# Optimization experiments

Measured on AMD Instinct MI355X. Metric: run time of the kernel, lower is better.

The kernel has to match this reference:

```python
import jax, jax.numpy as jnp
import numpy as np

N = 100_000      # nodes
E = 1_600_000    # edges (avg degree 16)
P = 100_000      # pos/neg sampled edges
L = 3            # GIN layers
D_IN = 128
D_H = 128
D_MLP = 512
D_PRED = D_H // 2
D_FIN = 1


def setup_inputs() -> dict:
    key = jax.random.key(0)
    ks = jax.random.split(key, 12)
    s_in = 1.0 / np.sqrt(D_IN)
    s_mlp = 1.0 / np.sqrt(D_MLP)
    s_h = 1.0 / np.sqrt(D_H)
    s_p = 1.0 / np.sqrt(D_PRED)
    return {
        "x":   jax.random.normal(ks[0], (N, D_IN), jnp.float32),
        "W1":  jax.random.normal(ks[1], (L, D_IN, D_MLP), jnp.float32) * s_in,
        "b1":  jnp.zeros((L, D_MLP), jnp.float32),
        "W2":  jax.random.normal(ks[2], (L, D_MLP, D_H), jnp.float32) * s_mlp,
        "b2":  jnp.zeros((L, D_H), jnp.float32),
        "Wp1": jax.random.normal(ks[3], (D_H, D_PRED), jnp.float32) * s_h,
        "bp1": jnp.zeros((D_PRED,), jnp.float32),
        "Wp2": jax.random.normal(ks[4], (D_PRED, D_FIN), jnp.float32) * s_p,
        "bp2": jnp.zeros((D_FIN,), jnp.float32),
        "edge_src": jax.random.randint(ks[5], (E,), 0, N),
        "edge_dst": jax.random.randint(ks[6], (E,), 0, N),
        "pos_src": jax.random.randint(ks[7], (P,), 0, N),
        "pos_dst": jax.random.randint(ks[8], (P,), 0, N),
        "neg_src": jax.random.randint(ks[9], (P,), 0, N),
        "neg_dst": jax.random.randint(ks[10], (P,), 0, N),
    }


def reference(x, W1, b1, W2, b2, Wp1, bp1, Wp2, bp2,
              edge_src, edge_dst, pos_src, pos_dst, neg_src, neg_dst):
    h = x
    for l in range(L):
        # GINConv 'sum': aggregate neighbor features src->dst, eps=0
        agg = jax.ops.segment_sum(h[edge_src], edge_dst, num_segments=N)
        z = jax.nn.relu((h + agg) @ W1[l] + b1[l])   # [N, D_MLP]
        h = z @ W2[l] + b2[l]                        # [N, D_H]
        h = jax.nn.relu(h)                           # outer ReLU in forward()

    def predict(src, dst):
        z = jax.nn.relu((h[src] * h[dst]) @ Wp1 + bp1)
        return z @ Wp2 + bp2                         # [P, D_FIN]

    h_pos = predict(pos_src, pos_dst)
    h_neg = predict(neg_src, neg_dst)
    return (h_pos, h_neg, h)
```

## Files before the change

kernel.cpp:

```cpp
#include <hip/hip_runtime.h>

typedef unsigned short ushort_t;

constexpr int NN = 100000;
constexpr int EE = 1600000;
constexpr int PP = 100000;
constexpr int DH = 128;
constexpr int DM = 512;

using frag_b16 = __attribute__((ext_vector_type(8))) short;
using frag_f32 = __attribute__((ext_vector_type(4))) float;

union FragU {
  ushort_t s[8];
  uint4 u;
  frag_b16 f;
};

__device__ inline void split_bf16(float x, ushort_t& hi, ushort_t& lo) {
  unsigned int bx = __float_as_uint(x);
  hi = (ushort_t)(bx >> 16);
  float hf = __uint_as_float(bx & 0xFFFF0000u);
  float r = x - hf;
  unsigned int br = __float_as_uint(r);
  unsigned int rb = br + 0x7FFFu + ((br >> 16) & 1u);
  lo = (ushort_t)(rb >> 16);
}

__device__ inline ushort_t rne_bf16(float x) {
  unsigned int u = __float_as_uint(x);
  unsigned int r = u + 0x7FFFu + ((u >> 16) & 1u);
  return (ushort_t)(r >> 16);
}

__device__ inline void bf2x(unsigned int u, float& a, float& b) {
  a = __uint_as_float(u << 16);
  b = __uint_as_float(u & 0xFFFF0000u);
}

__device__ inline void ldrec(const ushort_t* __restrict__ wp, int tile, int lane, FragU& f) {
  f.u = *(const uint4*)(wp + ((size_t)(tile * 64 + lane)) * 8);
}


__global__ void hist_kernel(const int* __restrict__ dst, int* __restrict__ deg) {
  int i = blockIdx.x * 256 + threadIdx.x;
  if (i < EE) atomicAdd(&deg[dst[i]], 1);
}

__global__ void scan1_kernel(const int* __restrict__ deg, int* __restrict__ inc,
                             int* __restrict__ bsum) {
  __shared__ int buf[2][512];
  int base = blockIdx.x * 512;
  for (int i = threadIdx.x; i < 512; i += 256) {
    int g = base + i;
    buf[0][i] = (g < NN) ? deg[g] : 0;
  }
  __syncthreads();
  int cur = 0;
  for (int off = 1; off < 512; off <<= 1) {
    int nxt = cur ^ 1;
    for (int i = threadIdx.x; i < 512; i += 256) {
      int v = buf[cur][i];
      if (i >= off) v += buf[cur][i - off];
      buf[nxt][i] = v;
    }
    __syncthreads();
    cur = nxt;
  }
  for (int i = threadIdx.x; i < 512; i += 256) {
    int g = base + i;
    if (g < NN) inc[g] = buf[cur][i];
  }
  if (threadIdx.x == 0) bsum[blockIdx.x] = buf[cur][511];
}

__global__ void scan2_kernel(int* __restrict__ bsum, int nb) {
  __shared__ int buf[2][256];
  int i = threadIdx.x;
  buf[0][i] = (i < nb) ? bsum[i] : 0;
  __syncthreads();
  int cur = 0;
  for (int off = 1; off < 256; off <<= 1) {
    int nxt = cur ^ 1;
    int v = buf[cur][i];
    if (i >= off) v += buf[cur][i - off];
    buf[nxt][i] = v;
    __syncthreads();
    cur = nxt;
  }
  if (i < nb) bsum[i] = (i == 0) ? 0 : buf[cur][i - 1];
}

__global__ void scan3_kernel(const int* __restrict__ inc, const int* __restrict__ deg,
                             const int* __restrict__ bsum,
                             int* __restrict__ row_off, int* __restrict__ cursor) {
  int i = blockIdx.x * 256 + threadIdx.x;
  if (i < NN) {
    int excl = inc[i] - deg[i] + bsum[i >> 9];
    row_off[i] = excl;
    cursor[i] = excl;
    if (i == NN - 1) row_off[NN] = excl + deg[i];
  }
}

constexpr int SC_NW = 8;
constexpr int SC_WND = (NN + SC_NW - 1) / SC_NW;
constexpr int SC_EPB = 8192;
constexpr int SC_CHUNKS = (EE + SC_EPB - 1) / SC_EPB;

__global__ __launch_bounds__(256) void scatter_kernel(const int* __restrict__ esrc,
                                                      const int* __restrict__ edst,
                                                      int* __restrict__ cursor,
                                                      int* __restrict__ csr) {
  const int w = blockIdx.x & (SC_NW - 1);
  const int chunk = blockIdx.x / SC_NW;
  const int lo = w * SC_WND;
  const int hi = lo + SC_WND;
  const int base = chunk * SC_EPB;
  #pragma unroll 4
  for (int it = 0; it < SC_EPB / 256; ++it) {
    int i = base + it * 256 + threadIdx.x;
    if (i < EE) {
      int d = edst[i];
      if (d >= lo && d < hi) {
        int p = atomicAdd(&cursor[d], 1);
        csr[p] = esrc[i];
      }
    }
  }
}

__global__ void pack_w1_kernel(const float* __restrict__ W1, ushort_t* __restrict__ wp) {
  int t = blockIdx.x * 256 + threadIdx.x;
  if (t >= 3 * 128 * 64) return;
  int lane = t & 63;
  int tile = t >> 6;
  int tk = tile & 3;
  int tn = (tile >> 2) & 31;
  int layer = tile >> 7;
  int n = tn * 16 + (lane & 15);
  int k0 = tk * 32 + (lane >> 4) * 8;
  const float* src = W1 + (size_t)layer * DH * DM;
  size_t dst = (size_t)t * 8;
  #pragma unroll
  for (int j = 0; j < 8; ++j) wp[dst + j] = rne_bf16(src[(size_t)(k0 + j) * DM + n]);
}

__global__ void pack_w2_kernel(const float* __restrict__ W2, ushort_t* __restrict__ wp) {
  int t = blockIdx.x * 256 + threadIdx.x;
  if (t >= 3 * 128 * 64) return;
  int lane = t & 63;
  int tile = t >> 6;
  int tk = tile & 15;
  int tn = (tile >> 4) & 7;
  int layer = tile >> 7;
  int n = tn * 16 + (lane & 15);
  int k0 = tk * 32 + (lane >> 4) * 8;
  const float* src = W2 + (size_t)layer * DM * DH;
  size_t dst = (size_t)t * 8;
  #pragma unroll
  for (int j = 0; j < 8; ++j) wp[dst + j] = rne_bf16(src[(size_t)(k0 + j) * DH + n]);
}

__global__ void cvt_bf16_kernel(const float* __restrict__ x, ushort_t* __restrict__ xb) {
  int i = blockIdx.x * 256 + threadIdx.x;
  if (i < NN * DH / 4) {
    float4 v = ((const float4*)x)[i];
    ushort4 o;
    o.x = rne_bf16(v.x); o.y = rne_bf16(v.y); o.z = rne_bf16(v.z); o.w = rne_bf16(v.w);
    ((ushort4*)xb)[i] = o;
  }
}

__global__ __launch_bounds__(256) void agg_kernel(const ushort_t* __restrict__ hbf,
                                                  const int* __restrict__ row_off,
                                                  const int* __restrict__ csr,
                                                  ushort_t* __restrict__ s_hi,
                                                  ushort_t* __restrict__ s_lo) {
  int t = blockIdx.x * 256 + threadIdx.x;
  int grp = t >> 4;
  int lane = t & 15;
  if (grp >= NN) return;
  const uint4* hp = (const uint4*)hbf;
  float acc[8];
  {
    uint4 v = hp[(size_t)grp * 16 + lane];
    bf2x(v.x, acc[0], acc[1]);
    bf2x(v.y, acc[2], acc[3]);
    bf2x(v.z, acc[4], acc[5]);
    bf2x(v.w, acc[6], acc[7]);
  }
  int e = row_off[grp];
  int e1 = row_off[grp + 1];
  for (; e + 1 < e1; e += 2) {
    uint4 a = hp[(size_t)csr[e] * 16 + lane];
    uint4 b = hp[(size_t)csr[e + 1] * 16 + lane];
    float f0, f1;
    bf2x(a.x, f0, f1); acc[0] += f0; acc[1] += f1;
    bf2x(a.y, f0, f1); acc[2] += f0; acc[3] += f1;
    bf2x(a.z, f0, f1); acc[4] += f0; acc[5] += f1;
    bf2x(a.w, f0, f1); acc[6] += f0; acc[7] += f1;
    bf2x(b.x, f0, f1); acc[0] += f0; acc[1] += f1;
    bf2x(b.y, f0, f1); acc[2] += f0; acc[3] += f1;
    bf2x(b.z, f0, f1); acc[4] += f0; acc[5] += f1;
    bf2x(b.w, f0, f1); acc[6] += f0; acc[7] += f1;
  }
  if (e < e1) {
    uint4 a = hp[(size_t)csr[e] * 16 + lane];
    float f0, f1;
    bf2x(a.x, f0, f1); acc[0] += f0; acc[1] += f1;
    bf2x(a.y, f0, f1); acc[2] += f0; acc[3] += f1;
    bf2x(a.z, f0, f1); acc[4] += f0; acc[5] += f1;
    bf2x(a.w, f0, f1); acc[6] += f0; acc[7] += f1;
  }
  unsigned int hw[4], lw[4];
  #pragma unroll
  for (int i = 0; i < 4; ++i) {
    ushort_t h0, l0, h1, l1;
    split_bf16(acc[2 * i], h0, l0);
    split_bf16(acc[2 * i + 1], h1, l1);
    hw[i] = (unsigned int)h0 | ((unsigned int)h1 << 16);
    lw[i] = (unsigned int)l0 | ((unsigned int)l1 << 16);
  }
  size_t o = (size_t)grp * DH + lane * 8;
  *(uint4*)(s_hi + o) = make_uint4(hw[0], hw[1], hw[2], hw[3]);
  *(uint4*)(s_lo + o) = make_uint4(lw[0], lw[1], lw[2], lw[3]);
}

__global__ __launch_bounds__(128) void mlp_kernel(
    const ushort_t* __restrict__ s_hi, const ushort_t* __restrict__ s_lo,
    const ushort_t* __restrict__ w1p, const float* __restrict__ b1s,
    const ushort_t* __restrict__ w2p, const float* __restrict__ b2s,
    float* __restrict__ hout_f32, ushort_t* __restrict__ hout_bf16) {
  __shared__ float zt[64 * 66];
  const int tid = threadIdx.x;
  const int wave = tid >> 6;
  const int lane = tid & 63;
  const int quad = lane >> 4;
  const int l15 = lane & 15;
  const int m_base = wave * 32;
  const int row0 = blockIdx.x * 64;

  frag_b16 a_hi[2][4], a_lo[2][4];
  #pragma unroll
  for (int ms = 0; ms < 2; ++ms) {
    int gr = row0 + m_base + ms * 16 + l15;
    if (gr >= NN) gr = NN - 1;
    #pragma unroll
    for (int tk = 0; tk < 4; ++tk) {
      size_t o = (size_t)gr * DH + tk * 32 + quad * 8;
      FragU uh, ul;
      uh.u = *(const uint4*)(s_hi + o);
      ul.u = *(const uint4*)(s_lo + o);
      a_hi[ms][tk] = uh.f;
      a_lo[ms][tk] = ul.f;
    }
  }

  frag_f32 hacc[2][8];
  #pragma unroll
  for (int ms = 0; ms < 2; ++ms)
    #pragma unroll
    for (int tn = 0; tn < 8; ++tn) hacc[ms][tn] = {0.f, 0.f, 0.f, 0.f};

  for (int ch = 0; ch < 8; ++ch) {
    frag_f32 za[2][4];
    #pragma unroll
    for (int ms = 0; ms < 2; ++ms)
      #pragma unroll
      for (int tn = 0; tn < 4; ++tn) za[ms][tn] = {0.f, 0.f, 0.f, 0.f};

    FragU wb[2][4];
    #pragma unroll
    for (int tn = 0; tn < 4; ++tn) ldrec(w1p, ch * 16 + tn * 4, lane, wb[0][tn]);
    #pragma unroll
    for (int tk = 0; tk < 4; ++tk) {
      int cur = tk & 1, nxt = cur ^ 1;
      if (tk < 3) {
        #pragma unroll
        for (int tn = 0; tn < 4; ++tn)
          ldrec(w1p, ch * 16 + tn * 4 + tk + 1, lane, wb[nxt][tn]);
      }
      #pragma unroll
      for (int tn = 0; tn < 4; ++tn) {
        #pragma unroll
        for (int ms = 0; ms < 2; ++ms) {
          za[ms][tn] = __builtin_amdgcn_mfma_f32_16x16x32_bf16(a_hi[ms][tk], wb[cur][tn].f,
                                                               za[ms][tn], 0, 0, 0);
          za[ms][tn] = __builtin_amdgcn_mfma_f32_16x16x32_bf16(a_lo[ms][tk], wb[cur][tn].f,
                                                               za[ms][tn], 0, 0, 0);
        }
      }
    }

    #pragma unroll
    for (int tn = 0; tn < 4; ++tn) {
      float b1v = b1s[ch * 64 + tn * 16 + l15];
      #pragma unroll
      for (int ms = 0; ms < 2; ++ms) {
        float z0 = fmaxf(za[ms][tn][0] + b1v, 0.f);
        float z1 = fmaxf(za[ms][tn][1] + b1v, 0.f);
        float z2 = fmaxf(za[ms][tn][2] + b1v, 0.f);
        float z3 = fmaxf(za[ms][tn][3] + b1v, 0.f);
        float* zp = &zt[(tn * 16 + l15) * 66 + m_base + ms * 16 + quad * 4];
        *(float2*)zp = make_float2(z0, z1);
        *(float2*)(zp + 2) = make_float2(z2, z3);
      }
    }

    #pragma unroll
    for (int kt = 0; kt < 2; ++kt) {
      int ktg = ch * 2 + kt;
      FragU wb2[8];
      #pragma unroll
      for (int tn = 0; tn < 8; ++tn) ldrec(w2p, tn * 16 + ktg, lane, wb2[tn]);
      FragU zh[2], zl[2];
      #pragma unroll
      for (int ms = 0; ms < 2; ++ms) {
        #pragma unroll
        for (int j = 0; j < 8; ++j) {
          int k = kt * 32 + quad * 8 + j;
          float v = zt[k * 66 + m_base + ms * 16 + l15];
          split_bf16(v, zh[ms].s[j], zl[ms].s[j]);
        }
      }
      #pragma unroll
      for (int tn = 0; tn < 8; ++tn) {
        #pragma unroll
        for (int ms = 0; ms < 2; ++ms) {
          hacc[ms][tn] = __builtin_amdgcn_mfma_f32_16x16x32_bf16(zh[ms].f, wb2[tn].f,
                                                                 hacc[ms][tn], 0, 0, 0);
          hacc[ms][tn] = __builtin_amdgcn_mfma_f32_16x16x32_bf16(zl[ms].f, wb2[tn].f,
                                                                 hacc[ms][tn], 0, 0, 0);
        }
      }
    }
  }

  #pragma unroll
  for (int tn = 0; tn < 8; ++tn) {
    int col = tn * 16 + l15;
    float b2v = b2s[col];
    #pragma unroll
    for (int ms = 0; ms < 2; ++ms) {
      #pragma unroll
      for (int r = 0; r < 4; ++r) {
        int gr = row0 + m_base + ms * 16 + quad * 4 + r;
        if (gr < NN) {
          float v = fmaxf(hacc[ms][tn][r] + b2v, 0.f);
          if (hout_f32) hout_f32[(size_t)gr * DH + col] = v;
          if (hout_bf16) hout_bf16[(size_t)gr * DH + col] = rne_bf16(v);
        }
      }
    }
  }
}

__global__ __launch_bounds__(256) void predict_kernel(
    const float* __restrict__ h, const int* __restrict__ psrc, const int* __restrict__ pdst,
    const int* __restrict__ nsrc, const int* __restrict__ ndst,
    const float* __restrict__ Wp1, const float* __restrict__ bp1,
    const float* __restrict__ Wp2, const float* __restrict__ bp2,
    float* __restrict__ out) {
  __shared__ float g_tile[64 * 132];
  const int tid = threadIdx.x;
  const int s0 = blockIdx.x * 64;

  #pragma unroll
  for (int i = 0; i < 8; ++i) {
    int idx = tid + i * 256;
    int smp = s0 + (idx >> 5);
    int c4 = (idx & 31) << 2;
    float4 g = make_float4(0.f, 0.f, 0.f, 0.f);
    if (smp < 2 * PP) {
      int si = (smp < PP) ? psrc[smp] : nsrc[smp - PP];
      int di = (smp < PP) ? pdst[smp] : ndst[smp - PP];
      float4 a = *(const float4*)(h + (size_t)si * DH + c4);
      float4 b = *(const float4*)(h + (size_t)di * DH + c4);
      g = make_float4(a.x * b.x, a.y * b.y, a.z * b.z, a.w * b.w);
    }
    *(float4*)(&g_tile[(idx >> 5) * 132 + c4]) = g;
  }
  __syncthreads();

  const int tr = (tid >> 4) << 2;
  const int tc = (tid & 15) << 2;
  float z[4][4];
  #pragma unroll
  for (int r = 0; r < 4; ++r)
    #pragma unroll
    for (int c = 0; c < 4; ++c) z[r][c] = 0.f;

  for (int k = 0; k < DH; ++k) {
    float4 w = *(const float4*)(Wp1 + ((size_t)k << 6) + tc);
    float a[4];
    #pragma unroll
    for (int r = 0; r < 4; ++r) a[r] = g_tile[(tr + r) * 132 + k];
    #pragma unroll
    for (int r = 0; r < 4; ++r) {
      z[r][0] = fmaf(a[r], w.x, z[r][0]);
      z[r][1] = fmaf(a[r], w.y, z[r][1]);
      z[r][2] = fmaf(a[r], w.z, z[r][2]);
      z[r][3] = fmaf(a[r], w.w, z[r][3]);
    }
  }

  float4 b1v = *(const float4*)(bp1 + tc);
  float4 w2v = *(const float4*)(Wp2 + tc);
  float part[4];
  #pragma unroll
  for (int r = 0; r < 4; ++r) {
    part[r] = fmaxf(z[r][0] + b1v.x, 0.f) * w2v.x +
              fmaxf(z[r][1] + b1v.y, 0.f) * w2v.y +
              fmaxf(z[r][2] + b1v.z, 0.f) * w2v.z +
              fmaxf(z[r][3] + b1v.w, 0.f) * w2v.w;
  }
  #pragma unroll
  for (int off = 1; off < 16; off <<= 1) {
    #pragma unroll
    for (int r = 0; r < 4; ++r) part[r] += __shfl_xor(part[r], off, 64);
  }
  if ((tid & 15) == 0) {
    float bias = bp2[0];
    #pragma unroll
    for (int r = 0; r < 4; ++r) {
      int smp = s0 + tr + r;
      if (smp < 2 * PP) out[smp] = part[r] + bias;
    }
  }
}

extern "C" void kernel_launch(void* const* d_in, const int* in_sizes, int n_in,
                              void* d_out, int out_size, void* d_ws, size_t ws_size,
                              hipStream_t stream) {
  const float* x   = (const float*)d_in[0];
  const float* W1  = (const float*)d_in[1];
  const float* b1  = (const float*)d_in[2];
  const float* W2  = (const float*)d_in[3];
  const float* b2  = (const float*)d_in[4];
  const float* Wp1 = (const float*)d_in[5];
  const float* bp1 = (const float*)d_in[6];
  const float* Wp2 = (const float*)d_in[7];
  const float* bp2 = (const float*)d_in[8];
  const int* esrc = (const int*)d_in[9];
  const int* edst = (const int*)d_in[10];
  const int* psrc = (const int*)d_in[11];
  const int* pdst = (const int*)d_in[12];
  const int* nsrc = (const int*)d_in[13];
  const int* ndst = (const int*)d_in[14];

  float* out = (float*)d_out;
  float* out_pred = out;
  float* hbuf = out + 2 * (size_t)PP;
  ushort_t* hbf = (ushort_t*)hbuf;

  char* w = (char*)d_ws;
  ushort_t* s_hi = (ushort_t*)w;
  ushort_t* s_lo = s_hi + (size_t)NN * DH;
  ushort_t* w1p  = s_lo + (size_t)NN * DH;
  ushort_t* w2p  = w1p + 3 * 128 * 64 * 8;
  int* row_off = (int*)(w2p + 3 * 128 * 64 * 8);
  int* csr     = row_off + (NN + 1);
  int* deg    = (int*)w;
  int* inc    = deg + NN;
  int* bsum   = inc + NN;
  int* cursor = bsum + 256;

  hipMemsetAsync(deg, 0, NN * sizeof(int), stream);
  hist_kernel<<<(EE + 255) / 256, 256, 0, stream>>>(edst, deg);
  scan1_kernel<<<(NN + 511) / 512, 256, 0, stream>>>(deg, inc, bsum);
  scan2_kernel<<<1, 256, 0, stream>>>(bsum, (NN + 511) / 512);
  scan3_kernel<<<(NN + 255) / 256, 256, 0, stream>>>(inc, deg, bsum, row_off, cursor);
  scatter_kernel<<<SC_CHUNKS * SC_NW, 256, 0, stream>>>(esrc, edst, cursor, csr);

  pack_w1_kernel<<<96, 256, 0, stream>>>(W1, w1p);
  pack_w2_kernel<<<96, 256, 0, stream>>>(W2, w2p);

  cvt_bf16_kernel<<<(NN * DH / 4 + 255) / 256, 256, 0, stream>>>(x, hbf);

  for (int l = 0; l < 3; ++l) {
    agg_kernel<<<(NN * 16 + 255) / 256, 256, 0, stream>>>(hbf, row_off, csr, s_hi, s_lo);
    mlp_kernel<<<(NN + 63) / 64, 128, 0, stream>>>(
        s_hi, s_lo,
        w1p + (size_t)l * 128 * 64 * 8, b1 + (size_t)l * DM,
        w2p + (size_t)l * 128 * 64 * 8, b2 + (size_t)l * DH,
        (l == 2) ? hbuf : nullptr, (l == 2) ? nullptr : hbf);
  }

  predict_kernel<<<(2 * PP + 63) / 64, 256, 0, stream>>>(
      hbuf, psrc, pdst, nsrc, ndst, Wp1, bp1, Wp2, bp2, out_pred);
}
```

Before: 887.7 us.

## Stage MLP weight tiles in LDS via global_load_lds with 4-wave blocks

```diff
diff --git a/kernel.cpp b/kernel.cpp
--- a/kernel.cpp
+++ b/kernel.cpp
@@ -38,8 +38,10 @@
   b = __uint_as_float(u & 0xFFFF0000u);
 }
 
-__device__ inline void ldrec(const ushort_t* __restrict__ wp, int tile, int lane, FragU& f) {
-  f.u = *(const uint4*)(wp + ((size_t)(tile * 64 + lane)) * 8);
+__device__ inline void g2l16(const ushort_t* __restrict__ g, ushort_t* l) {
+  __builtin_amdgcn_global_load_lds(
+      (const __attribute__((address_space(1))) void*)g,
+      (__attribute__((address_space(3))) void*)l, 16, 0, 0);
 }
 
 
@@ -152,11 +154,11 @@
   if (t >= 3 * 128 * 64) return;
   int lane = t & 63;
   int tile = t >> 6;
-  int tk = tile & 15;
-  int tn = (tile >> 4) & 7;
+  int tn = tile & 7;
+  int ktg = (tile >> 3) & 15;
   int layer = tile >> 7;
   int n = tn * 16 + (lane & 15);
-  int k0 = tk * 32 + (lane >> 4) * 8;
+  int k0 = ktg * 32 + (lane >> 4) * 8;
   const float* src = W2 + (size_t)layer * DM * DH;
   size_t dst = (size_t)t * 8;
   #pragma unroll
@@ -228,19 +230,21 @@
   *(uint4*)(s_lo + o) = make_uint4(lw[0], lw[1], lw[2], lw[3]);
 }
 
-__global__ __launch_bounds__(128) void mlp_kernel(
+__global__ __launch_bounds__(256, 2) void mlp_kernel(
     const ushort_t* __restrict__ s_hi, const ushort_t* __restrict__ s_lo,
     const ushort_t* __restrict__ w1p, const float* __restrict__ b1s,
     const ushort_t* __restrict__ w2p, const float* __restrict__ b2s,
     float* __restrict__ hout_f32, ushort_t* __restrict__ hout_bf16) {
-  __shared__ float zt[64 * 66];
+  __shared__ ushort_t wA[8 * 512];
+  __shared__ ushort_t wB[8 * 512];
+  __shared__ float zt[32 * 130];
   const int tid = threadIdx.x;
   const int wave = tid >> 6;
   const int lane = tid & 63;
   const int quad = lane >> 4;
   const int l15 = lane & 15;
   const int m_base = wave * 32;
-  const int row0 = blockIdx.x * 64;
+  const int row0 = blockIdx.x * 128;
 
   frag_b16 a_hi[2][4], a_lo[2][4];
   #pragma unroll
@@ -264,78 +268,74 @@
     #pragma unroll
     for (int tn = 0; tn < 8; ++tn) hacc[ms][tn] = {0.f, 0.f, 0.f, 0.f};
 
-  for (int ch = 0; ch < 8; ++ch) {
-    frag_f32 za[2][4];
+  for (int ch = 0; ch < 16; ++ch) {
+    #pragma unroll
+    for (int i = 0; i < 2; ++i)
+      g2l16(w1p + ((size_t)(ch * 512 + i * 256 + tid)) * 8, wA + (i * 256 + tid) * 8);
+    #pragma unroll
+    for (int i = 0; i < 2; ++i)
+      g2l16(w2p + ((size_t)(ch * 512 + i * 256 + tid)) * 8, wB + (i * 256 + tid) * 8);
+    __syncthreads();
+
+    frag_f32 za[2][2];
     #pragma unroll
     for (int ms = 0; ms < 2; ++ms)
       #pragma unroll
-      for (int tn = 0; tn < 4; ++tn) za[ms][tn] = {0.f, 0.f, 0.f, 0.f};
-
-    FragU wb[2][4];
-    #pragma unroll
-    for (int tn = 0; tn < 4; ++tn) ldrec(w1p, ch * 16 + tn * 4, lane, wb[0][tn]);
+      for (int tn = 0; tn < 2; ++tn) za[ms][tn] = {0.f, 0.f, 0.f, 0.f};
+
     #pragma unroll
     for (int tk = 0; tk < 4; ++tk) {
-      int cur = tk & 1, nxt = cur ^ 1;
-      if (tk < 3) {
-        #pragma unroll
-        for (int tn = 0; tn < 4; ++tn)
-          ldrec(w1p, ch * 16 + tn * 4 + tk + 1, lane, wb[nxt][tn]);
-      }
-      #pragma unroll
-      for (int tn = 0; tn < 4; ++tn) {
+      #pragma unroll
+      for (int tn = 0; tn < 2; ++tn) {
+        FragU wv;
+        wv.u = *(const uint4*)(wA + (tn * 4 + tk) * 512 + lane * 8);
         #pragma unroll
         for (int ms = 0; ms < 2; ++ms) {
-          za[ms][tn] = __builtin_amdgcn_mfma_f32_16x16x32_bf16(a_hi[ms][tk], wb[cur][tn].f,
+          za[ms][tn] = __builtin_amdgcn_mfma_f32_16x16x32_bf16(a_hi[ms][tk], wv.f,
                                                                za[ms][tn], 0, 0, 0);
-          za[ms][tn] = __builtin_amdgcn_mfma_f32_16x16x32_bf16(a_lo[ms][tk], wb[cur][tn].f,
+          za[ms][tn] = __builtin_amdgcn_mfma_f32_16x16x32_bf16(a_lo[ms][tk], wv.f,
                                                                za[ms][tn], 0, 0, 0);
         }
       }
     }
 
     #pragma unroll
-    for (int tn = 0; tn < 4; ++tn) {
-      float b1v = b1s[ch * 64 + tn * 16 + l15];
+    for (int tn = 0; tn < 2; ++tn) {
+      float b1v = b1s[ch * 32 + tn * 16 + l15];
       #pragma unroll
       for (int ms = 0; ms < 2; ++ms) {
         float z0 = fmaxf(za[ms][tn][0] + b1v, 0.f);
         float z1 = fmaxf(za[ms][tn][1] + b1v, 0.f);
         float z2 = fmaxf(za[ms][tn][2] + b1v, 0.f);
         float z3 = fmaxf(za[ms][tn][3] + b1v, 0.f);
-        float* zp = &zt[(tn * 16 + l15) * 66 + m_base + ms * 16 + quad * 4];
+        float* zp = &zt[(tn * 16 + l15) * 130 + m_base + ms * 16 + quad * 4];
         *(float2*)zp = make_float2(z0, z1);
         *(float2*)(zp + 2) = make_float2(z2, z3);
       }
     }
 
-    #pragma unroll
-    for (int kt = 0; kt < 2; ++kt) {
-      int ktg = ch * 2 + kt;
-      FragU wb2[8];
-      #pragma unroll
-      for (int tn = 0; tn < 8; ++tn) ldrec(w2p, tn * 16 + ktg, lane, wb2[tn]);
-      FragU zh[2], zl[2];
+    FragU zh[2], zl[2];
+    #pragma unroll
+    for (int ms = 0; ms < 2; ++ms) {
+      #pragma unroll
+      for (int j = 0; j < 8; ++j) {
+        float v = zt[(quad * 8 + j) * 130 + m_base + ms * 16 + l15];
+        split_bf16(v, zh[ms].s[j], zl[ms].s[j]);
+      }
+    }
+    #pragma unroll
+    for (int tn = 0; tn < 8; ++tn) {
+      FragU wv;
+      wv.u = *(const uint4*)(wB + tn * 512 + lane * 8);
       #pragma unroll
       for (int ms = 0; ms < 2; ++ms) {
-        #pragma unroll
-        for (int j = 0; j < 8; ++j) {
-          int k = kt * 32 + quad * 8 + j;
-          float v = zt[k * 66 + m_base + ms * 16 + l15];
-          split_bf16(v, zh[ms].s[j], zl[ms].s[j]);
-        }
-      }
-      #pragma unroll
-      for (int tn = 0; tn < 8; ++tn) {
-        #pragma unroll
-        for (int ms = 0; ms < 2; ++ms) {
-          hacc[ms][tn] = __builtin_amdgcn_mfma_f32_16x16x32_bf16(zh[ms].f, wb2[tn].f,
-                                                                 hacc[ms][tn], 0, 0, 0);
-          hacc[ms][tn] = __builtin_amdgcn_mfma_f32_16x16x32_bf16(zl[ms].f, wb2[tn].f,
-                                                                 hacc[ms][tn], 0, 0, 0);
-        }
-      }
-    }
+        hacc[ms][tn] = __builtin_amdgcn_mfma_f32_16x16x32_bf16(zh[ms].f, wv.f,
+                                                               hacc[ms][tn], 0, 0, 0);
+        hacc[ms][tn] = __builtin_amdgcn_mfma_f32_16x16x32_bf16(zl[ms].f, wv.f,
+                                                               hacc[ms][tn], 0, 0, 0);
+      }
+    }
+    __syncthreads();
   }
 
   #pragma unroll
@@ -481,7 +481,7 @@
 
   for (int l = 0; l < 3; ++l) {
     agg_kernel<<<(NN * 16 + 255) / 256, 256, 0, stream>>>(hbf, row_off, csr, s_hi, s_lo);
-    mlp_kernel<<<(NN + 63) / 64, 128, 0, stream>>>(
+    mlp_kernel<<<(NN + 127) / 128, 256, 0, stream>>>(
         s_hi, s_lo,
         w1p + (size_t)l * 128 * 64 * 8, b1 + (size_t)l * DM,
         w2p + (size_t)l * 128 * 64 * 8, b2 + (size_t)l * DH,
```

After: 798.3 us. -10.1%, faster.
